# Optimization experiments

Hardware: AMD Instinct MI355X
Metric: run time of the kernel (lower is better)

## Reference

```python
import jax, jax.numpy as jnp
import numpy as np

EPS_REG = 0.05      # epsilon (entropic regularization), learn_epsilon=False
NUM_ITERS = 20      # Sinkhorn iterations
MESH_ITERS = 3      # MESH sharpening iterations


def setup_inputs() -> dict:
    key = jax.random.key(0)
    k1, k2, k3, k4 = jax.random.split(key, 4)
    B, K, M, D = 2048, 64, 64, 256
    slots_q = jax.random.normal(k1, (B, K, D), dtype=jnp.float32)
    slots_r = jax.random.normal(k2, (B, M, D), dtype=jnp.float32)
    mask_q = jnp.ones((B, K), dtype=jnp.float32)
    mask_r = jnp.ones((B, M), dtype=jnp.float32)
    W1 = jax.random.normal(k3, (D, D), dtype=jnp.float32) * (1.0 / np.sqrt(D))
    b1 = jnp.zeros((D,), dtype=jnp.float32)
    W2 = jax.random.normal(k4, (D, D), dtype=jnp.float32) * (1.0 / np.sqrt(D))
    b2 = jnp.zeros((D,), dtype=jnp.float32)
    return {"slots_q": slots_q, "slots_r": slots_r, "mask_q": mask_q,
            "mask_r": mask_r, "W1": W1, "b1": b1, "W2": W2, "b2": b2}


def _cost_proj(x, W1, b1, W2, b2):
    h = jax.nn.relu(jnp.einsum('bnd,de->bne', x, W1) + b1)
    return jnp.einsum('bnd,de->bne', h, W2) + b2


def _cdist(q, r):
    # Euclidean pairwise distance: [B,K,M]
    q2 = jnp.sum(q * q, axis=-1)                      # [B,K]
    r2 = jnp.sum(r * r, axis=-1)                      # [B,M]
    qr = jnp.einsum('bkd,bmd->bkm', q, r)             # [B,K,M]
    d2 = q2[:, :, None] + r2[:, None, :] - 2.0 * qr
    return jnp.sqrt(jnp.clip(d2, 0.0))


def _sinkhorn(C, mask_q, mask_r):
    log_K = -C / EPS_REG
    log_K = log_K + jnp.log(jnp.clip(mask_q, 1e-8))[:, :, None]
    log_K = log_K + jnp.log(jnp.clip(mask_r, 1e-8))[:, None, :]
    B, K, M = C.shape
    la0 = jnp.zeros((B, K, 1), dtype=C.dtype)
    lb0 = jnp.zeros((B, 1, M), dtype=C.dtype)

    def body(i, carry):
        la, lb = carry
        la = -jax.nn.logsumexp(log_K + lb, axis=2, keepdims=True)
        lb = -jax.nn.logsumexp(log_K + la, axis=1, keepdims=True)
        return (la, lb)

    la, lb = jax.lax.fori_loop(0, NUM_ITERS, body, (la0, lb0))
    return jnp.exp(log_K + la + lb)


def _mesh(T):
    def body(i, T):
        Ts = T * T
        Ts = Ts / (jnp.sum(Ts, axis=-1, keepdims=True) + 1e-8)
        Ts = Ts / (jnp.sum(Ts, axis=-2, keepdims=True) + 1e-8)
        return Ts
    return jax.lax.fori_loop(0, MESH_ITERS, body, T)


def reference(slots_q, slots_r, mask_q, mask_r, W1, b1, W2, b2):
    q_proj = _cost_proj(slots_q, W1, b1, W2, b2)
    r_proj = _cost_proj(slots_r, W1, b1, W2, b2)
    C = _cdist(q_proj, r_proj)                        # [B,K,M]
    T = _sinkhorn(C, mask_q, mask_r)                  # [B,K,M]
    T_hard = _mesh(T)
    transport_cost = jnp.sum(T_hard * C, axis=(-1, -2))   # [B]
    similarity = jax.nn.sigmoid(-transport_cost)           # [B]
    return similarity, T_hard, C, transport_cost
```

## Files before the change

### kernel.cpp

```cpp
#include <hip/hip_runtime.h>


typedef __attribute__((ext_vector_type(8))) short s16x8;
typedef __attribute__((ext_vector_type(4))) float f32x4;

#define OFF_T  2048
#define OFF_C  (2048 + 2048 * 4096)
#define OFF_TC (2048 + 2 * 2048 * 4096)

__device__ __forceinline__ unsigned short f2bf(float x) {
  unsigned u = __builtin_bit_cast(unsigned, x);
  u += 0x7fffu + ((u >> 16) & 1u);
  return (unsigned short)(u >> 16);
}
__device__ __forceinline__ float bf2f(unsigned short h) {
  return __builtin_bit_cast(float, ((unsigned)h) << 16);
}

#define MFMA16(a, b, c) __builtin_amdgcn_mfma_f32_16x16x32_bf16((a), (b), (c), 0, 0, 0)

__global__ void __launch_bounds__(256)
prep_w_kernel(const float* __restrict__ W1, const float* __restrict__ W2,
              short* __restrict__ W1t, short* __restrict__ W2t) {
  int i = blockIdx.x * 256 + threadIdx.x;
  int d = i >> 8, e = i & 255;
  W1t[e * 256 + d] = (short)f2bf(W1[i]);
  W2t[e * 256 + d] = (short)f2bf(W2[i]);
}

__device__ __forceinline__ void gemm_kloop(const short* __restrict__ wb,
                                           const char* sm, int abase0, int asw,
                                           int koff0, f32x4 (&acc)[8][4]) {
  s16x8 bwc[4], bwn[4];
#pragma unroll
  for (int nf = 0; nf < 4; ++nf) bwc[nf] = *(const s16x8*)(wb + nf * 4096);
#pragma unroll
  for (int ks = 0; ks < 8; ++ks) {
    if (ks < 7) {
#pragma unroll
      for (int nf = 0; nf < 4; ++nf)
        bwn[nf] = *(const s16x8*)(wb + nf * 4096 + (ks + 1) * 32);
    }
    const int ko = (ks * 64 + koff0) ^ asw;
    s16x8 af[8];
#pragma unroll
    for (int rf = 0; rf < 8; ++rf)
      af[rf] = *(const s16x8*)(sm + rf * 8192 + abase0 + ko);
#pragma unroll
    for (int rf = 0; rf < 8; ++rf)
#pragma unroll
      for (int nf = 0; nf < 4; ++nf)
        acc[rf][nf] = MFMA16(af[rf], bwc[nf], acc[rf][nf]);
    if (ks < 7) {
#pragma unroll
      for (int nf = 0; nf < 4; ++nf) bwc[nf] = bwn[nf];
    }
  }
}

__global__ void __launch_bounds__(256, 2)
proj_cost_kernel(const float* __restrict__ slots_q, const float* __restrict__ slots_r,
                 const short* __restrict__ W1t, const short* __restrict__ W2t,
                 const float* __restrict__ b1, const float* __restrict__ b2,
                 float* __restrict__ out) {
  __shared__ char smem[65536];
  float* nbuf = (float*)smem;

  const int b    = blockIdx.x;
  const int tid  = threadIdx.x;
  const int wv   = tid >> 6;
  const int lane = tid & 63;
  const int l15  = lane & 15;
  const int lhi  = lane >> 4;

  {
    const float* sq = slots_q + (size_t)b * 16384;
    const float* sr = slots_r + (size_t)b * 16384;
#pragma unroll
    for (int i = 0; i < 32; ++i) {
      int idx4 = tid + 256 * i;
      int row = idx4 >> 6;
      int colb = (idx4 & 63) * 8;
      const float* src = (i < 16) ? (sq + idx4 * 4) : (sr + idx4 * 4 - 16384);
      float4 v = *(const float4*)src;
      unsigned lo = (unsigned)f2bf(v.x) | ((unsigned)f2bf(v.y) << 16);
      unsigned hi = (unsigned)f2bf(v.z) | ((unsigned)f2bf(v.w) << 16);
      *(uint2*)(smem + row * 512 + (colb ^ ((row & 7) << 4))) = make_uint2(lo, hi);
    }
  }
  __syncthreads();

  const int abase0 = l15 * 512;
  const int asw    = (l15 & 7) << 4;
  const int koff0  = lhi * 16;
  const short* wb1 = W1t + (wv * 64 + l15) * 256 + lhi * 8;
  const short* wb2 = W2t + (wv * 64 + l15) * 256 + lhi * 8;

  float b1v[4], b2v[4];
#pragma unroll
  for (int nf = 0; nf < 4; ++nf) {
    b1v[nf] = b1[wv * 64 + nf * 16 + l15];
    b2v[nf] = b2[wv * 64 + nf * 16 + l15];
  }

  const f32x4 z4 = {0.f, 0.f, 0.f, 0.f};
  f32x4 acc[8][4];

#pragma unroll
  for (int rf = 0; rf < 8; ++rf)
#pragma unroll
    for (int nf = 0; nf < 4; ++nf) acc[rf][nf] = z4;
  gemm_kloop(wb1, smem, abase0, asw, koff0, acc);
  __syncthreads();
#pragma unroll
  for (int rf = 0; rf < 8; ++rf)
#pragma unroll
    for (int nf = 0; nf < 4; ++nf)
#pragma unroll
      for (int j = 0; j < 4; ++j) {
        int row = rf * 16 + lhi * 4 + j;
        int colb = (wv * 64 + nf * 16 + l15) * 2;
        *(unsigned short*)(smem + row * 512 + (colb ^ ((row & 7) << 4))) =
            f2bf(fmaxf(acc[rf][nf][j] + b1v[nf], 0.0f));
      }
  __syncthreads();

#pragma unroll
  for (int rf = 0; rf < 8; ++rf)
#pragma unroll
    for (int nf = 0; nf < 4; ++nf) acc[rf][nf] = z4;
  gemm_kloop(wb2, smem, abase0, asw, koff0, acc);
  __syncthreads();

  float p2[8][4];
#pragma unroll
  for (int rf = 0; rf < 8; ++rf)
#pragma unroll
    for (int j = 0; j < 4; ++j) {
      float s = 0.0f;
#pragma unroll
      for (int nf = 0; nf < 4; ++nf) {
        unsigned short h = f2bf(acc[rf][nf][j] + b2v[nf]);
        int row = rf * 16 + lhi * 4 + j;
        int colb = (wv * 64 + nf * 16 + l15) * 2;
        *(unsigned short*)(smem + row * 512 + (colb ^ ((row & 7) << 4))) = h;
        float f = bf2f(h);
        s += f * f;
      }
      p2[rf][j] = s;
    }
#pragma unroll
  for (int d = 1; d < 16; d <<= 1)
#pragma unroll
    for (int rf = 0; rf < 8; ++rf)
#pragma unroll
      for (int j = 0; j < 4; ++j) p2[rf][j] += __shfl_xor(p2[rf][j], d);
  __syncthreads();

  f32x4 accC[4];
#pragma unroll
  for (int n = 0; n < 4; ++n) accC[n] = z4;
#pragma unroll
  for (int ks = 0; ks < 8; ++ks) {
    const int ko = (ks * 64 + koff0) ^ asw;
    s16x8 aQ = *(const s16x8*)(smem + wv * 8192 + abase0 + ko);
#pragma unroll
    for (int n = 0; n < 4; ++n) {
      s16x8 bR = *(const s16x8*)(smem + 32768 + n * 8192 + abase0 + ko);
      accC[n] = MFMA16(aQ, bR, accC[n]);
    }
  }
  __syncthreads();

  if (l15 == 0) {
#pragma unroll
    for (int rf = 0; rf < 8; ++rf) {
      f32x4 v = {p2[rf][0], p2[rf][1], p2[rf][2], p2[rf][3]};
      *(f32x4*)(nbuf + wv * 128 + rf * 16 + lhi * 4) = v;
    }
  }
  __syncthreads();

  f32x4 nq = z4;
#pragma unroll
  for (int w = 0; w < 4; ++w)
    nq += *(const f32x4*)(nbuf + w * 128 + wv * 16 + lhi * 4);
  float nR[4];
#pragma unroll
  for (int n = 0; n < 4; ++n) {
    float s = 0.0f;
#pragma unroll
    for (int w = 0; w < 4; ++w) s += nbuf[w * 128 + 64 + n * 16 + l15];
    nR[n] = s;
  }

  float* Cb = out + OFF_C + (size_t)b * 4096;
#pragma unroll
  for (int n = 0; n < 4; ++n)
#pragma unroll
    for (int j = 0; j < 4; ++j) {
      float d2 = nq[j] + nR[n] - 2.0f * accC[n][j];
      Cb[(wv * 16 + lhi * 4 + j) * 64 + n * 16 + l15] = sqrtf(fmaxf(d2, 0.0f));
    }
}

__global__ void __launch_bounds__(256, 4)
sinkhorn_solve(const float* __restrict__ mask_r, float* __restrict__ out) {
  __shared__ float tile[64 * 65];
  __shared__ float u_arr[64], w_arr[64], red[4];

  const int b    = blockIdx.x;
  const int tid  = threadIdx.x;
  const int wv   = tid >> 6;
  const int lane = tid & 63;
  const int rk   = tid >> 2;
  const int g    = tid & 3;
  const int e0   = g * 16;

  const float* Cb = out + OFF_C + (size_t)b * 4096;

#pragma unroll
  for (int i = 0; i < 16; ++i) {
    int idx = tid + 256 * i;
    tile[(idx >> 6) * 65 + (idx & 63)] = Cb[idx];
  }
  if (tid < 64) w_arr[tid] = __logf(fmaxf(mask_r[(size_t)b * 64 + tid], 1e-8f));
  __syncthreads();

  float cn[16], cc[16];
#pragma unroll
  for (int i = 0; i < 16; ++i) {
    cn[i] = tile[rk * 65 + e0 + i] * -20.0f;
    cc[i] = tile[(e0 + i) * 65 + rk] * -20.0f;
  }

  for (int it = 0; it < 20; ++it) {
    {
      float v[16];
#pragma unroll
      for (int i = 0; i < 16; ++i) v[i] = cn[i] + w_arr[e0 + i];
      float mx = v[0];
#pragma unroll
      for (int i = 1; i < 16; ++i) mx = fmaxf(mx, v[i]);
      float s = 0.0f;
#pragma unroll
      for (int i = 0; i < 16; ++i) s += __expf(v[i] - mx);
#pragma unroll
      for (int d = 1; d < 4; d <<= 1) {
        float mo = __shfl_xor(mx, d), so = __shfl_xor(s, d);
        float nm = fmaxf(mx, mo);
        s = s * __expf(mx - nm) + so * __expf(mo - nm);
        mx = nm;
      }
      if (g == 0) u_arr[rk] = -(mx + __logf(s));
    }
    __syncthreads();
    {
      float v[16];
#pragma unroll
      for (int i = 0; i < 16; ++i) v[i] = cc[i] + u_arr[e0 + i];
      float mx = v[0];
#pragma unroll
      for (int i = 1; i < 16; ++i) mx = fmaxf(mx, v[i]);
      float s = 0.0f;
#pragma unroll
      for (int i = 0; i < 16; ++i) s += __expf(v[i] - mx);
#pragma unroll
      for (int d = 1; d < 4; d <<= 1) {
        float mo = __shfl_xor(mx, d), so = __shfl_xor(s, d);
        float nm = fmaxf(mx, mo);
        s = s * __expf(mx - nm) + so * __expf(mo - nm);
        mx = nm;
      }
      if (g == 0) w_arr[rk] = -(mx + __logf(s));
    }
    __syncthreads();
  }

  float t[16];
  {
    float uk = u_arr[rk];
#pragma unroll
    for (int i = 0; i < 16; ++i) t[i] = __expf(cn[i] + uk + w_arr[e0 + i]);
  }
  for (int it = 0; it < 3; ++it) {
    if (it > 0) {
      __syncthreads();
#pragma unroll
      for (int i = 0; i < 16; ++i) t[i] = tile[rk * 65 + e0 + i];
    }
    float s = 0.0f;
#pragma unroll
    for (int i = 0; i < 16; ++i) { t[i] *= t[i]; s += t[i]; }
    s += __shfl_xor(s, 1); s += __shfl_xor(s, 2);
    float inv = 1.0f / (s + 1e-8f);
#pragma unroll
    for (int i = 0; i < 16; ++i) tile[rk * 65 + e0 + i] = t[i] * inv;
    __syncthreads();
    float tc[16]; float cs = 0.0f;
#pragma unroll
    for (int i = 0; i < 16; ++i) { tc[i] = tile[(e0 + i) * 65 + rk]; cs += tc[i]; }
    cs += __shfl_xor(cs, 1); cs += __shfl_xor(cs, 2);
    inv = 1.0f / (cs + 1e-8f);
#pragma unroll
    for (int i = 0; i < 16; ++i) tile[(e0 + i) * 65 + rk] = tc[i] * inv;
  }
  __syncthreads();

  {
    float part = 0.0f;
#pragma unroll
    for (int i = 0; i < 16; ++i)
      part += tile[rk * 65 + e0 + i] * (cn[i] * -0.05f);
#pragma unroll
    for (int d = 1; d < 64; d <<= 1) part += __shfl_xor(part, d);
    if (lane == 0) red[wv] = part;
  }
  __syncthreads();
  if (tid == 0) {
    float tc = red[0] + red[1] + red[2] + red[3];
    out[OFF_TC + b] = tc;
    out[b] = 1.0f / (1.0f + __expf(tc));
  }
  {
    float* Tout = out + OFF_T + (size_t)b * 4096;
#pragma unroll
    for (int i = 0; i < 16; ++i) {
      int idx = tid + 256 * i;
      Tout[idx] = tile[(idx >> 6) * 65 + (idx & 63)];
    }
  }
}

extern "C" void kernel_launch(void* const* d_in, const int* in_sizes, int n_in,
                              void* d_out, int out_size, void* d_ws, size_t ws_size,
                              hipStream_t stream) {
  const float* slots_q = (const float*)d_in[0];
  const float* slots_r = (const float*)d_in[1];
  const float* mask_r = (const float*)d_in[3];
  const float* W1 = (const float*)d_in[4];
  const float* b1 = (const float*)d_in[5];
  const float* W2 = (const float*)d_in[6];
  const float* b2 = (const float*)d_in[7];

  short* W1t = (short*)d_ws;
  short* W2t = W1t + 65536;

  prep_w_kernel<<<256, 256, 0, stream>>>(W1, W2, W1t, W2t);
  proj_cost_kernel<<<2048, 256, 0, stream>>>(slots_q, slots_r, W1t, W2t, b1, b2,
                                             (float*)d_out);
  sinkhorn_solve<<<2048, 256, 0, stream>>>(mask_r, (float*)d_out);
}
```

Before: 292.9 us.

## Split projection per slot set and fuse cdist into Sinkhorn kernel

Projection now runs as 4096 blocks, one per batch and slot set (q or r), using half the shared memory and a higher occupancy bound. Projected features are written as bf16 to workspace along with row norms. The pairwise-distance GEMM moves into the Sinkhorn kernel, which computes C on chip, writes it out, and feeds it straight into the iterations without re-reading C from global memory. This adds a bf16 workspace round trip for the projections and depends on the workspace being large enough, otherwise it falls back to the old path.

New measurement: 317.0 us. +8.2%, slower.

```diff
diff --git a/kernel.cpp b/kernel.cpp
--- a/kernel.cpp
+++ b/kernel.cpp
@@ -7,6 +7,8 @@
 #define OFF_T  2048
 #define OFF_C  (2048 + 2048 * 4096)
 #define OFF_TC (2048 + 2 * 2048 * 4096)
+
+#define WS_NEED 135528448ull
 
 __device__ __forceinline__ unsigned short f2bf(float x) {
   unsigned u = __builtin_bit_cast(unsigned, x);
@@ -28,9 +30,10 @@
   W2t[e * 256 + d] = (short)f2bf(W2[i]);
 }
 
+template <int RF>
 __device__ __forceinline__ void gemm_kloop(const short* __restrict__ wb,
                                            const char* sm, int abase0, int asw,
-                                           int koff0, f32x4 (&acc)[8][4]) {
+                                           int koff0, f32x4 (&acc)[RF][4]) {
   s16x8 bwc[4], bwn[4];
 #pragma unroll
   for (int nf = 0; nf < 4; ++nf) bwc[nf] = *(const s16x8*)(wb + nf * 4096);
@@ -42,18 +45,139 @@
         bwn[nf] = *(const s16x8*)(wb + nf * 4096 + (ks + 1) * 32);
     }
     const int ko = (ks * 64 + koff0) ^ asw;
-    s16x8 af[8];
-#pragma unroll
-    for (int rf = 0; rf < 8; ++rf)
+    s16x8 af[RF];
+#pragma unroll
+    for (int rf = 0; rf < RF; ++rf)
       af[rf] = *(const s16x8*)(sm + rf * 8192 + abase0 + ko);
 #pragma unroll
-    for (int rf = 0; rf < 8; ++rf)
+    for (int rf = 0; rf < RF; ++rf)
 #pragma unroll
       for (int nf = 0; nf < 4; ++nf)
         acc[rf][nf] = MFMA16(af[rf], bwc[nf], acc[rf][nf]);
     if (ks < 7) {
 #pragma unroll
       for (int nf = 0; nf < 4; ++nf) bwc[nf] = bwn[nf];
+    }
+  }
+}
+
+__global__ void __launch_bounds__(256, 3)
+proj_kernel(const float* __restrict__ slots_q, const float* __restrict__ slots_r,
+            const short* __restrict__ W1t, const short* __restrict__ W2t,
+            const float* __restrict__ b1, const float* __restrict__ b2,
+            short* __restrict__ Pws, float* __restrict__ norms_g) {
+  __shared__ char smem[32768 + 1024];
+  float* nbuf = (float*)(smem + 32768);
+
+  const int bb   = blockIdx.x;
+  const int tid  = threadIdx.x;
+  const int wv   = tid >> 6;
+  const int lane = tid & 63;
+  const int l15  = lane & 15;
+  const int lhi  = lane >> 4;
+
+  {
+    const float* src = ((bb & 1) ? slots_r : slots_q) + (size_t)(bb >> 1) * 16384;
+#pragma unroll
+    for (int i = 0; i < 16; ++i) {
+      int idx4 = tid + 256 * i;
+      int row = idx4 >> 6;
+      int colb = (idx4 & 63) * 8;
+      float4 v = *(const float4*)(src + idx4 * 4);
+      unsigned lo = (unsigned)f2bf(v.x) | ((unsigned)f2bf(v.y) << 16);
+      unsigned hi = (unsigned)f2bf(v.z) | ((unsigned)f2bf(v.w) << 16);
+      *(uint2*)(smem + row * 512 + (colb ^ ((row & 7) << 4))) = make_uint2(lo, hi);
+    }
+  }
+  __syncthreads();
+
+  const int abase0 = l15 * 512;
+  const int asw    = (l15 & 7) << 4;
+  const int koff0  = lhi * 16;
+  const short* wb1 = W1t + (wv * 64 + l15) * 256 + lhi * 8;
+  const short* wb2 = W2t + (wv * 64 + l15) * 256 + lhi * 8;
+
+  float b1v[4], b2v[4];
+#pragma unroll
+  for (int nf = 0; nf < 4; ++nf) {
+    b1v[nf] = b1[wv * 64 + nf * 16 + l15];
+    b2v[nf] = b2[wv * 64 + nf * 16 + l15];
+  }
+
+  const f32x4 z4 = {0.f, 0.f, 0.f, 0.f};
+  f32x4 acc[4][4];
+
+#pragma unroll
+  for (int rf = 0; rf < 4; ++rf)
+#pragma unroll
+    for (int nf = 0; nf < 4; ++nf) acc[rf][nf] = z4;
+  gemm_kloop<4>(wb1, smem, abase0, asw, koff0, acc);
+  __syncthreads();
+#pragma unroll
+  for (int rf = 0; rf < 4; ++rf)
+#pragma unroll
+    for (int nf = 0; nf < 4; ++nf)
+#pragma unroll
+      for (int j = 0; j < 4; ++j) {
+        int row = rf * 16 + lhi * 4 + j;
+        int colb = (wv * 64 + nf * 16 + l15) * 2;
+        *(unsigned short*)(smem + row * 512 + (colb ^ ((row & 7) << 4))) =
+            f2bf(fmaxf(acc[rf][nf][j] + b1v[nf], 0.0f));
+      }
+  __syncthreads();
+
+#pragma unroll
+  for (int rf = 0; rf < 4; ++rf)
+#pragma unroll
+    for (int nf = 0; nf < 4; ++nf) acc[rf][nf] = z4;
+  gemm_kloop<4>(wb2, smem, abase0, asw, koff0, acc);
+  __syncthreads();
+
+  float p2[4][4];
+#pragma unroll
+  for (int rf = 0; rf < 4; ++rf)
+#pragma unroll
+    for (int j = 0; j < 4; ++j) {
+      float s = 0.0f;
+#pragma unroll
+      for (int nf = 0; nf < 4; ++nf) {
+        unsigned short h = f2bf(acc[rf][nf][j] + b2v[nf]);
+        int row = rf * 16 + lhi * 4 + j;
+        int colb = (wv * 64 + nf * 16 + l15) * 2;
+        *(unsigned short*)(smem + row * 512 + (colb ^ ((row & 7) << 4))) = h;
+        float f = bf2f(h);
+        s += f * f;
+      }
+      p2[rf][j] = s;
+    }
+#pragma unroll
+  for (int d = 1; d < 16; d <<= 1)
+#pragma unroll
+    for (int rf = 0; rf < 4; ++rf)
+#pragma unroll
+      for (int j = 0; j < 4; ++j) p2[rf][j] += __shfl_xor(p2[rf][j], d);
+  if (l15 == 0) {
+#pragma unroll
+    for (int rf = 0; rf < 4; ++rf) {
+      f32x4 v = {p2[rf][0], p2[rf][1], p2[rf][2], p2[rf][3]};
+      *(f32x4*)(nbuf + wv * 64 + rf * 16 + lhi * 4) = v;
+    }
+  }
+  __syncthreads();
+
+  {
+    short* Pg = Pws + (size_t)bb * 16384;
+#pragma unroll
+    for (int i = 0; i < 8; ++i) {
+      int idx = tid + 256 * i;
+      int row = idx >> 5;
+      int colb = (idx & 31) * 16;
+      s16x8 v = *(const s16x8*)(smem + row * 512 + (colb ^ ((row & 7) << 4)));
+      *(s16x8*)(Pg + idx * 8) = v;
+    }
+    if (tid < 64) {
+      float s = nbuf[tid] + nbuf[64 + tid] + nbuf[128 + tid] + nbuf[192 + tid];
+      norms_g[bb * 64 + tid] = s;
     }
   }
 }
@@ -110,7 +234,7 @@
   for (int rf = 0; rf < 8; ++rf)
 #pragma unroll
     for (int nf = 0; nf < 4; ++nf) acc[rf][nf] = z4;
-  gemm_kloop(wb1, smem, abase0, asw, koff0, acc);
+  gemm_kloop<8>(wb1, smem, abase0, asw, koff0, acc);
   __syncthreads();
 #pragma unroll
   for (int rf = 0; rf < 8; ++rf)
@@ -129,7 +253,7 @@
   for (int rf = 0; rf < 8; ++rf)
 #pragma unroll
     for (int nf = 0; nf < 4; ++nf) acc[rf][nf] = z4;
-  gemm_kloop(wb2, smem, abase0, asw, koff0, acc);
+  gemm_kloop<8>(wb2, smem, abase0, asw, koff0, acc);
   __syncthreads();
 
   float p2[8][4];
@@ -204,28 +328,92 @@
     }
 }
 
+template <int MODE>
 __global__ void __launch_bounds__(256, 4)
-sinkhorn_solve(const float* __restrict__ mask_r, float* __restrict__ out) {
-  __shared__ float tile[64 * 65];
+sinkhorn_solve_k(const float* __restrict__ mask_r, const short* __restrict__ Pws,
+                 const float* __restrict__ norms_g, float* __restrict__ out) {
+  __shared__ char bsm[32768];
   __shared__ float u_arr[64], w_arr[64], red[4];
+  float* tile = (float*)bsm;
 
   const int b    = blockIdx.x;
   const int tid  = threadIdx.x;
   const int wv   = tid >> 6;
   const int lane = tid & 63;
+  const int l15  = lane & 15;
+  const int lhi  = lane >> 4;
   const int rk   = tid >> 2;
   const int g    = tid & 3;
   const int e0   = g * 16;
 
-  const float* Cb = out + OFF_C + (size_t)b * 4096;
-
-#pragma unroll
-  for (int i = 0; i < 16; ++i) {
-    int idx = tid + 256 * i;
-    tile[(idx >> 6) * 65 + (idx & 63)] = Cb[idx];
-  }
   if (tid < 64) w_arr[tid] = __logf(fmaxf(mask_r[(size_t)b * 64 + tid], 1e-8f));
-  __syncthreads();
+
+  if (MODE == 0) {
+    const float* Cb = out + OFF_C + (size_t)b * 4096;
+#pragma unroll
+    for (int i = 0; i < 16; ++i) {
+      int idx = tid + 256 * i;
+      tile[(idx >> 6) * 65 + (idx & 63)] = Cb[idx];
+    }
+    __syncthreads();
+  } else {
+    const short* Pq = Pws + (size_t)(2 * b) * 16384;
+    const short* Pr = Pws + (size_t)(2 * b + 1) * 16384;
+    s16x8 af[8];
+#pragma unroll
+    for (int ks = 0; ks < 8; ++ks)
+      af[ks] = *(const s16x8*)(Pq + (wv * 16 + l15) * 256 + ks * 32 + lhi * 8);
+#pragma unroll
+    for (int i = 0; i < 8; ++i) {
+      int idx = tid + 256 * i;
+      int row = idx >> 5;
+      int colb = (idx & 31) * 16;
+      *(s16x8*)(bsm + row * 512 + (colb ^ ((row & 7) << 4))) =
+          *(const s16x8*)(Pr + idx * 8);
+    }
+    float q2v[4], r2v[4];
+#pragma unroll
+    for (int j = 0; j < 4; ++j)
+      q2v[j] = norms_g[2 * b * 64 + wv * 16 + lhi * 4 + j];
+#pragma unroll
+    for (int n = 0; n < 4; ++n)
+      r2v[n] = norms_g[(2 * b + 1) * 64 + n * 16 + l15];
+    __syncthreads();
+
+    const f32x4 z4 = {0.f, 0.f, 0.f, 0.f};
+    f32x4 accC[4];
+#pragma unroll
+    for (int n = 0; n < 4; ++n) accC[n] = z4;
+    const int asw = (l15 & 7) << 4;
+#pragma unroll
+    for (int ks = 0; ks < 8; ++ks) {
+      const int ko = ks * 64 + lhi * 16;
+#pragma unroll
+      for (int n = 0; n < 4; ++n) {
+        int row = n * 16 + l15;
+        s16x8 bR = *(const s16x8*)(bsm + row * 512 + (ko ^ asw));
+        accC[n] = MFMA16(af[ks], bR, accC[n]);
+      }
+    }
+    __syncthreads();
+
+#pragma unroll
+    for (int n = 0; n < 4; ++n)
+#pragma unroll
+      for (int j = 0; j < 4; ++j) {
+        int k = wv * 16 + lhi * 4 + j;
+        int m = n * 16 + l15;
+        float d2 = q2v[j] + r2v[n] - 2.0f * accC[n][j];
+        tile[k * 65 + m] = sqrtf(fmaxf(d2, 0.0f));
+      }
+    __syncthreads();
+    float* Cb = out + OFF_C + (size_t)b * 4096;
+#pragma unroll
+    for (int i = 0; i < 16; ++i) {
+      int idx = tid + 256 * i;
+      Cb[idx] = tile[(idx >> 6) * 65 + (idx & 63)];
+    }
+  }
 
   float cn[16], cc[16];
 #pragma unroll
@@ -345,9 +533,19 @@
 
   short* W1t = (short*)d_ws;
   short* W2t = W1t + 65536;
+  float* norms = (float*)((char*)d_ws + 262144);
+  short* Pws = (short*)((char*)d_ws + 1310720);
 
   prep_w_kernel<<<256, 256, 0, stream>>>(W1, W2, W1t, W2t);
-  proj_cost_kernel<<<2048, 256, 0, stream>>>(slots_q, slots_r, W1t, W2t, b1, b2,
-                                             (float*)d_out);
-  sinkhorn_solve<<<2048, 256, 0, stream>>>(mask_r, (float*)d_out);
-}
+  if (ws_size >= WS_NEED) {
+    proj_kernel<<<4096, 256, 0, stream>>>(slots_q, slots_r, W1t, W2t, b1, b2,
+                                          Pws, norms);
+    sinkhorn_solve_k<1><<<2048, 256, 0, stream>>>(mask_r, Pws, norms,
+                                                  (float*)d_out);
+  } else {
+    proj_cost_kernel<<<2048, 256, 0, stream>>>(slots_q, slots_r, W1t, W2t, b1,
+                                               b2, (float*)d_out);
+    sinkhorn_solve_k<0><<<2048, 256, 0, stream>>>(mask_r, nullptr, nullptr,
+                                                  (float*)d_out);
+  }
+}
```
